# Optimization experiments

Measured on AMD Instinct MI355X. Metric: run time of the kernel, lower is better.

Reference implementation:

```python
import jax, jax.numpy as jnp
import numpy as np

# Gemma3 layer 0 (sliding-window layer -> local RoPE)
H = 8          # query heads
KVH = 4        # kv heads
DH = 256       # head dim
WINDOW = 1024  # sliding window
THETA_LOCAL = 10000.0
SCALE = 256.0 ** -0.5  # query_pre_attn_scalar**-0.5
EPS = 1e-6


def setup_inputs() -> dict:
    key = jax.random.key(0)
    ks = jax.random.split(key, 8)
    B, S, D = 1, 4096, 2560
    return {
        "hidden_states": jax.random.normal(ks[0], (B, S, D), jnp.float32),
        "attention_mask": jnp.ones((B, S), jnp.int32),
        "position_ids": jnp.broadcast_to(jnp.arange(S, dtype=jnp.int64), (B, S)),
        "wq": jax.random.normal(ks[1], (D, H * DH), jnp.float32) * 0.02,
        "wk": jax.random.normal(ks[2], (D, KVH * DH), jnp.float32) * 0.02,
        "wv": jax.random.normal(ks[3], (D, KVH * DH), jnp.float32) * 0.02,
        "wo": jax.random.normal(ks[4], (H * DH, D), jnp.float32) * 0.02,
        "q_norm_w": jnp.zeros((DH,), jnp.float32),  # Gemma RMSNorm uses (1 + w)
        "k_norm_w": jnp.zeros((DH,), jnp.float32),
    }


def _rms_norm(x, w):
    # Gemma-style RMSNorm over head_dim: x/rms * (1 + w)
    var = jnp.mean(jnp.square(x), axis=-1, keepdims=True)
    return x * jax.lax.rsqrt(var + EPS) * (1.0 + w)


def _rotate_half(x):
    x1, x2 = jnp.split(x, 2, axis=-1)
    return jnp.concatenate([-x2, x1], axis=-1)


def _rope(pos):
    # local RoPE (rope_type 'default', theta = rope_local_base_freq)
    inv_freq = 1.0 / (THETA_LOCAL ** (jnp.arange(0, DH, 2, dtype=jnp.float32) / DH))
    freqs = pos.astype(jnp.float32)[..., None] * inv_freq  # [B,S,DH/2]
    emb = jnp.concatenate([freqs, freqs], axis=-1)         # [B,S,DH]
    return jnp.cos(emb), jnp.sin(emb)


def reference(hidden_states, attention_mask, position_ids, wq, wk, wv, wo, q_norm_w, k_norm_w):
    B, S, D = hidden_states.shape
    # projections -> [B, heads, S, DH]
    q = (hidden_states @ wq).reshape(B, S, H, DH).transpose(0, 2, 1, 3)
    k = (hidden_states @ wk).reshape(B, S, KVH, DH).transpose(0, 2, 1, 3)
    v = (hidden_states @ wv).reshape(B, S, KVH, DH).transpose(0, 2, 1, 3)

    # per-head q/k RMSNorm (Gemma3)
    q = _rms_norm(q, q_norm_w)
    k = _rms_norm(k, k_norm_w)

    # RoPE
    cos, sin = _rope(position_ids)           # [B,S,DH]
    cos, sin = cos[:, None], sin[:, None]    # broadcast over heads
    q = q * cos + _rotate_half(q) * sin
    k = k * cos + _rotate_half(k) * sin

    # GQA: repeat kv heads
    rep = H // KVH
    k = jnp.repeat(k, rep, axis=1)
    v = jnp.repeat(v, rep, axis=1)

    # causal + sliding-window mask, combined with padding mask
    qi = jnp.arange(S)[:, None]
    ki = jnp.arange(S)[None, :]
    sw_mask = (ki <= qi) & (qi - ki < WINDOW)               # [S,S]
    pad = attention_mask.astype(bool)[:, None, None, :]     # [B,1,1,S]
    mask = sw_mask[None, None] & pad

    scores = jnp.einsum("bhqd,bhkd->bhqk", q, k) * SCALE
    scores = jnp.where(mask, scores, jnp.finfo(scores.dtype).min)
    probs = jax.nn.softmax(scores, axis=-1)

    out = jnp.einsum("bhqk,bhkd->bhqd", probs, v)            # [B,H,S,DH]
    out = out.transpose(0, 2, 1, 3).reshape(B, S, H * DH)
    return out @ wo
```

## Files before the change

kernel.cpp:

```cpp
#include <hip/hip_runtime.h>
#include <stdint.h>
#include <math.h>

typedef __bf16 bf16_t;
typedef __bf16 bf16x8 __attribute__((ext_vector_type(8)));
typedef __bf16 bf16x4 __attribute__((ext_vector_type(4)));
typedef float f32x4 __attribute__((ext_vector_type(4)));

#define GLD_LDS16(g, l)                                             \
    __builtin_amdgcn_global_load_lds(                               \
        (const __attribute__((address_space(1))) void*)(g),         \
        (__attribute__((address_space(3))) void*)(l), 16, 0, 0)

#define WAITV(N) asm volatile("s_waitcnt vmcnt(" #N ")" ::: "memory")
#define BARRIER() do { __builtin_amdgcn_sched_barrier(0);           \
                       __builtin_amdgcn_s_barrier();                \
                       __builtin_amdgcn_sched_barrier(0); } while (0)

__global__ __launch_bounds__(256)
void conv_bf16(const float* __restrict__ in, bf16_t* __restrict__ out, int n4)
{
    int i = blockIdx.x * 256 + threadIdx.x;
    if (i >= n4) return;
    float4 v = ((const float4*)in)[i];
    bf16x4 o = { (bf16_t)v.x, (bf16_t)v.y, (bf16_t)v.z, (bf16_t)v.w };
    ((bf16x4*)out)[i] = o;
}

__global__ __launch_bounds__(256)
void transpose_h(const float* __restrict__ in, bf16_t* __restrict__ out,
                 int R, int C)
{
    __shared__ float t[64][65];
    const int r0 = blockIdx.y * 64, c0 = blockIdx.x * 64;
#pragma unroll
    for (int i = 0; i < 16; ++i) {
        int f = threadIdx.x + i * 256;
        int r = f >> 6, c = f & 63;
        t[r][c] = in[(size_t)(r0 + r) * C + c0 + c];
    }
    __syncthreads();
#pragma unroll
    for (int i = 0; i < 16; ++i) {
        int f = threadIdx.x + i * 256;
        int r = f >> 6, c = f & 63;
        out[(size_t)(c0 + r) * R + r0 + c] = (bf16_t)t[c][r];
    }
}

__global__ __launch_bounds__(256)
void rope_tables(float* __restrict__ ct, float* __restrict__ st)
{
    int t = blockIdx.x * 256 + threadIdx.x;
    int s = t >> 7, j = t & 127;
    double inv = exp2((double)j * (-13.28771237954945 / 128.0));
    double ang = fmod((double)s * inv, 6.283185307179586476925286766559);
    ct[t] = (float)cos(ang);
    st[t] = (float)sin(ang);
}

__global__ __launch_bounds__(512, 2)
void gemm1(const bf16_t* __restrict__ A, const bf16_t* __restrict__ Bh,
           bf16_t* __restrict__ qb, bf16_t* __restrict__ kb,
           bf16_t* __restrict__ vt)
{
    __shared__ __attribute__((aligned(16))) char smem[131072];
    const int tid = threadIdx.x, lane = tid & 63, wid = tid >> 6;
    const int g = lane >> 4, c16 = lane & 15;
    const int wm = wid >> 2, wn = wid & 3;
    const int m0 = blockIdx.y * 256, n0 = blockIdx.x * 256;
    const int swz = c16 & 7;
    const int NT = 40;

    f32x4 acc[8][4];
#pragma unroll
    for (int m = 0; m < 8; ++m)
#pragma unroll
        for (int n = 0; n < 4; ++n) acc[m][n] = (f32x4)(0.f);

    auto STAGE_A = [&](int dbuf, int kt, int half) {
#pragma unroll
        for (int pl = 0; pl < 2; ++pl) {
            int c = pl * 512 + tid;
            int row = c >> 3, b = c & 7;
            GLD_LDS16(A + (size_t)(m0 + half * 128 + row) * 2560 + kt * 64
                        + ((b ^ (row & 7)) << 3),
                      smem + dbuf * 65536 + half * 16384
                        + (pl * 512 + wid * 64) * 16);
        }
    };
    auto STAGE_B = [&](int dbuf, int kt, int qp) {
#pragma unroll
        for (int pl = 0; pl < 2; ++pl) {
            int c = pl * 512 + tid;
            int u = c >> 3, b = c & 7;
            int row = ((u >> 5) << 6) + qp * 32 + (u & 31);
            int u0 = pl * 64 + wid * 8;
            int row0 = ((u0 >> 5) << 6) + qp * 32 + (u0 & 31);
            GLD_LDS16(Bh + (size_t)(n0 + row) * 2560 + kt * 64
                        + ((b ^ (row & 7)) << 3),
                      smem + dbuf * 65536 + 32768 + row0 * 128);
        }
    };

    STAGE_A(0, 0, 0); STAGE_A(0, 0, 1); STAGE_B(0, 0, 0); STAGE_B(0, 0, 1);
    WAITV(2);
    BARRIER();

    for (int t = 0; t < NT; ++t) {
        const int buf = t & 1, nbuf = buf ^ 1;
        const char* Ab = smem + buf * 65536;
        const char* Bb = smem + buf * 65536 + 32768;
        auto rdA = [&](int m, int kk) {
            return *(const bf16x8*)(Ab + (wm * 128 + m * 16 + c16) * 128
                                       + (((kk * 4 + g) ^ swz) << 4));
        };
        auto rdB = [&](int n, int kk) {
            return *(const bf16x8*)(Bb + (wn * 64 + n * 16 + c16) * 128
                                       + (((kk * 4 + g) ^ swz) << 4));
        };
        bf16x8 a[8], b0, b1, b2, b3;

#pragma unroll
        for (int m = 0; m < 8; ++m) a[m] = rdA(m, 0);
        b0 = rdB(0, 0); b1 = rdB(1, 0);
        if (t + 1 < NT) STAGE_A(nbuf, t + 1, 0);
        BARRIER();
        __builtin_amdgcn_s_setprio(1);
#pragma unroll
        for (int m = 0; m < 8; ++m) {
            acc[m][0] = __builtin_amdgcn_mfma_f32_16x16x32_bf16(a[m], b0, acc[m][0], 0, 0, 0);
            acc[m][1] = __builtin_amdgcn_mfma_f32_16x16x32_bf16(a[m], b1, acc[m][1], 0, 0, 0);
        }
        __builtin_amdgcn_s_setprio(0);
        if (t + 1 < NT) { WAITV(2); } else { WAITV(0); }
        BARRIER();

        b2 = rdB(2, 0); b3 = rdB(3, 0);
        if (t + 1 < NT) STAGE_A(nbuf, t + 1, 1);
        BARRIER();
        __builtin_amdgcn_s_setprio(1);
#pragma unroll
        for (int m = 0; m < 8; ++m) {
            acc[m][2] = __builtin_amdgcn_mfma_f32_16x16x32_bf16(a[m], b2, acc[m][2], 0, 0, 0);
            acc[m][3] = __builtin_amdgcn_mfma_f32_16x16x32_bf16(a[m], b3, acc[m][3], 0, 0, 0);
        }
        __builtin_amdgcn_s_setprio(0);
        BARRIER();

#pragma unroll
        for (int m = 0; m < 8; ++m) a[m] = rdA(m, 1);
        b0 = rdB(0, 1); b1 = rdB(1, 1);
        if (t + 1 < NT) STAGE_B(nbuf, t + 1, 0);
        BARRIER();
        __builtin_amdgcn_s_setprio(1);
#pragma unroll
        for (int m = 0; m < 8; ++m) {
            acc[m][0] = __builtin_amdgcn_mfma_f32_16x16x32_bf16(a[m], b0, acc[m][0], 0, 0, 0);
            acc[m][1] = __builtin_amdgcn_mfma_f32_16x16x32_bf16(a[m], b1, acc[m][1], 0, 0, 0);
        }
        __builtin_amdgcn_s_setprio(0);
        BARRIER();

        b2 = rdB(2, 1); b3 = rdB(3, 1);
        if (t + 1 < NT) STAGE_B(nbuf, t + 1, 1);
        BARRIER();
        __builtin_amdgcn_s_setprio(1);
#pragma unroll
        for (int m = 0; m < 8; ++m) {
            acc[m][2] = __builtin_amdgcn_mfma_f32_16x16x32_bf16(a[m], b2, acc[m][2], 0, 0, 0);
            acc[m][3] = __builtin_amdgcn_mfma_f32_16x16x32_bf16(a[m], b3, acc[m][3], 0, 0, 0);
        }
        __builtin_amdgcn_s_setprio(0);
        if (t + 1 < NT) WAITV(2);
        BARRIER();
    }

    if (n0 < 2048) {
#pragma unroll
        for (int m = 0; m < 8; ++m)
#pragma unroll
            for (int n = 0; n < 4; ++n) {
                int col = n0 + wn * 64 + n * 16 + c16;
                int rowb = m0 + wm * 128 + m * 16 + g * 4;
#pragma unroll
                for (int r = 0; r < 4; ++r)
                    qb[(size_t)(rowb + r) * 2048 + col] = (bf16_t)acc[m][n][r];
            }
    } else if (n0 < 3072) {
#pragma unroll
        for (int m = 0; m < 8; ++m)
#pragma unroll
            for (int n = 0; n < 4; ++n) {
                int col = n0 + wn * 64 + n * 16 + c16 - 2048;
                int rowb = m0 + wm * 128 + m * 16 + g * 4;
#pragma unroll
                for (int r = 0; r < 4; ++r)
                    kb[(size_t)(rowb + r) * 1024 + col] = (bf16_t)acc[m][n][r];
            }
    } else {
#pragma unroll
        for (int m = 0; m < 8; ++m)
#pragma unroll
            for (int n = 0; n < 4; ++n) {
                int d = n0 + wn * 64 + n * 16 + c16 - 3072;
                int rowb = m0 + wm * 128 + m * 16 + g * 4;
                int kvh_ = d >> 8, dd = d & 255;
                int kt = rowb >> 5, key = rowb & 31;
                bf16x4 hv;
#pragma unroll
                for (int r = 0; r < 4; ++r) hv[r] = (bf16_t)acc[m][n][r];
                size_t off = (size_t)kvh_ * 1048576 + (size_t)kt * 8192
                           + dd * 32 + (((key >> 3) ^ (dd & 3)) << 3) + (key & 7);
                *(bf16x4*)(vt + off) = hv;
            }
    }
}

__global__ __launch_bounds__(512, 2)
void gemm2p(const bf16_t* __restrict__ A, const bf16_t* __restrict__ Bh,
            float* __restrict__ C)
{
    __shared__ __attribute__((aligned(16))) char smem[131072];
    const int tid = threadIdx.x, lane = tid & 63, wid = tid >> 6;
    const int g = lane >> 4, c16 = lane & 15;
    const int wm = wid >> 2, wn = wid & 3;
    const int m0 = blockIdx.y * 256, n0 = blockIdx.x * 256;
    const int swz = c16 & 7;
    const int NT = 32;

    f32x4 acc[8][4];
#pragma unroll
    for (int m = 0; m < 8; ++m)
#pragma unroll
        for (int n = 0; n < 4; ++n) acc[m][n] = (f32x4)(0.f);

    auto STAGE_A = [&](int dbuf, int kt, int half) {
#pragma unroll
        for (int pl = 0; pl < 2; ++pl) {
            int c = pl * 512 + tid;
            int row = c >> 3, b = c & 7;
            GLD_LDS16(A + (size_t)(m0 + half * 128 + row) * 2048 + kt * 64
                        + ((b ^ (row & 7)) << 3),
                      smem + dbuf * 65536 + half * 16384
                        + (pl * 512 + wid * 64) * 16);
        }
    };
    auto STAGE_B = [&](int dbuf, int kt, int qp) {
#pragma unroll
        for (int pl = 0; pl < 2; ++pl) {
            int c = pl * 512 + tid;
            int u = c >> 3, b = c & 7;
            int row = ((u >> 5) << 6) + qp * 32 + (u & 31);
            int u0 = pl * 64 + wid * 8;
            int row0 = ((u0 >> 5) << 6) + qp * 32 + (u0 & 31);
            GLD_LDS16(Bh + (size_t)(n0 + row) * 2048 + kt * 64
                        + ((b ^ (row & 7)) << 3),
                      smem + dbuf * 65536 + 32768 + row0 * 128);
        }
    };

    STAGE_A(0, 0, 0); STAGE_A(0, 0, 1); STAGE_B(0, 0, 0); STAGE_B(0, 0, 1);
    WAITV(2);
    BARRIER();

    for (int t = 0; t < NT; ++t) {
        const int buf = t & 1, nbuf = buf ^ 1;
        const char* Ab = smem + buf * 65536;
        const char* Bb = smem + buf * 65536 + 32768;
        auto rdA = [&](int m, int kk) {
            return *(const bf16x8*)(Ab + (wm * 128 + m * 16 + c16) * 128
                                       + (((kk * 4 + g) ^ swz) << 4));
        };
        auto rdB = [&](int n, int kk) {
            return *(const bf16x8*)(Bb + (wn * 64 + n * 16 + c16) * 128
                                       + (((kk * 4 + g) ^ swz) << 4));
        };
        bf16x8 a[8], b0, b1, b2, b3;

#pragma unroll
        for (int m = 0; m < 8; ++m) a[m] = rdA(m, 0);
        b0 = rdB(0, 0); b1 = rdB(1, 0);
        if (t + 1 < NT) STAGE_A(nbuf, t + 1, 0);
        BARRIER();
        __builtin_amdgcn_s_setprio(1);
#pragma unroll
        for (int m = 0; m < 8; ++m) {
            acc[m][0] = __builtin_amdgcn_mfma_f32_16x16x32_bf16(a[m], b0, acc[m][0], 0, 0, 0);
            acc[m][1] = __builtin_amdgcn_mfma_f32_16x16x32_bf16(a[m], b1, acc[m][1], 0, 0, 0);
        }
        __builtin_amdgcn_s_setprio(0);
        if (t + 1 < NT) { WAITV(2); } else { WAITV(0); }
        BARRIER();

        b2 = rdB(2, 0); b3 = rdB(3, 0);
        if (t + 1 < NT) STAGE_A(nbuf, t + 1, 1);
        BARRIER();
        __builtin_amdgcn_s_setprio(1);
#pragma unroll
        for (int m = 0; m < 8; ++m) {
            acc[m][2] = __builtin_amdgcn_mfma_f32_16x16x32_bf16(a[m], b2, acc[m][2], 0, 0, 0);
            acc[m][3] = __builtin_amdgcn_mfma_f32_16x16x32_bf16(a[m], b3, acc[m][3], 0, 0, 0);
        }
        __builtin_amdgcn_s_setprio(0);
        BARRIER();

#pragma unroll
        for (int m = 0; m < 8; ++m) a[m] = rdA(m, 1);
        b0 = rdB(0, 1); b1 = rdB(1, 1);
        if (t + 1 < NT) STAGE_B(nbuf, t + 1, 0);
        BARRIER();
        __builtin_amdgcn_s_setprio(1);
#pragma unroll
        for (int m = 0; m < 8; ++m) {
            acc[m][0] = __builtin_amdgcn_mfma_f32_16x16x32_bf16(a[m], b0, acc[m][0], 0, 0, 0);
            acc[m][1] = __builtin_amdgcn_mfma_f32_16x16x32_bf16(a[m], b1, acc[m][1], 0, 0, 0);
        }
        __builtin_amdgcn_s_setprio(0);
        BARRIER();

        b2 = rdB(2, 1); b3 = rdB(3, 1);
        if (t + 1 < NT) STAGE_B(nbuf, t + 1, 1);
        BARRIER();
        __builtin_amdgcn_s_setprio(1);
#pragma unroll
        for (int m = 0; m < 8; ++m) {
            acc[m][2] = __builtin_amdgcn_mfma_f32_16x16x32_bf16(a[m], b2, acc[m][2], 0, 0, 0);
            acc[m][3] = __builtin_amdgcn_mfma_f32_16x16x32_bf16(a[m], b3, acc[m][3], 0, 0, 0);
        }
        __builtin_amdgcn_s_setprio(0);
        if (t + 1 < NT) WAITV(2);
        BARRIER();
    }

#pragma unroll
    for (int m = 0; m < 8; ++m)
#pragma unroll
        for (int n = 0; n < 4; ++n) {
            int col = n0 + wn * 64 + n * 16 + c16;
            int rowb = m0 + wm * 128 + m * 16 + g * 4;
#pragma unroll
            for (int r = 0; r < 4; ++r)
                C[(size_t)(rowb + r) * 2560 + col] = acc[m][n][r];
        }
}

__global__ __launch_bounds__(256)
void norm_q(bf16_t* __restrict__ qb, const float* __restrict__ w,
            const float* __restrict__ ct, const float* __restrict__ st)
{
    const int s = blockIdx.x, t = threadIdx.x;
    const int h = t >> 5, l = t & 31;
    bf16_t* base = qb + (size_t)s * 2048 + h * 256 + l * 8;
    bf16x8 hv = *(const bf16x8*)base;
    float x[8], ss = 0.f;
#pragma unroll
    for (int j = 0; j < 8; ++j) { x[j] = (float)hv[j]; ss += x[j] * x[j]; }
#pragma unroll
    for (int mk = 1; mk < 32; mk <<= 1) ss += __shfl_xor(ss, mk);
    const float rs = rsqrtf(ss * (1.f / 256.f) + 1e-6f);
    float4 w0 = *(const float4*)(w + l * 8);
    float4 w1 = *(const float4*)(w + l * 8 + 4);
    float wa[8] = { w0.x, w0.y, w0.z, w0.w, w1.x, w1.y, w1.z, w1.w };
    float xn[8];
#pragma unroll
    for (int j = 0; j < 8; ++j) xn[j] = x[j] * rs * (1.f + wa[j]);
    const int d0 = (l * 8) & 127;
    float4 c0 = *(const float4*)(ct + s * 128 + d0);
    float4 c1 = *(const float4*)(ct + s * 128 + d0 + 4);
    float4 s0 = *(const float4*)(st + s * 128 + d0);
    float4 s1 = *(const float4*)(st + s * 128 + d0 + 4);
    float cc[8] = { c0.x, c0.y, c0.z, c0.w, c1.x, c1.y, c1.z, c1.w };
    float sn[8] = { s0.x, s0.y, s0.z, s0.w, s1.x, s1.y, s1.z, s1.w };
    const bool upper = (l >= 16);
    bf16x8 oh;
#pragma unroll
    for (int j = 0; j < 8; ++j) {
        float pn = __shfl_xor(xn[j], 16);
        float rot = upper ? pn : -pn;
        oh[j] = (bf16_t)(xn[j] * cc[j] + rot * sn[j]);
    }
    *(bf16x8*)base = oh;
}

__global__ __launch_bounds__(256)
void norm_k(const bf16_t* __restrict__ kraw, bf16_t* __restrict__ kb2,
            const float* __restrict__ w, const float* __restrict__ ct,
            const float* __restrict__ st)
{
    const int s = blockIdx.x, t = threadIdx.x;
    const int h = t >> 6, l = t & 63;
    const bf16_t* base = kraw + (size_t)s * 1024 + h * 256 + l * 4;
    bf16x4 hv = *(const bf16x4*)base;
    float x[4], ss = 0.f;
#pragma unroll
    for (int j = 0; j < 4; ++j) { x[j] = (float)hv[j]; ss += x[j] * x[j]; }
#pragma unroll
    for (int mk = 1; mk < 64; mk <<= 1) ss += __shfl_xor(ss, mk);
    const float rs = rsqrtf(ss * (1.f / 256.f) + 1e-6f);
    float4 w0 = *(const float4*)(w + l * 4);
    float wa[4] = { w0.x, w0.y, w0.z, w0.w };
    float xn[4];
#pragma unroll
    for (int j = 0; j < 4; ++j) xn[j] = x[j] * rs * (1.f + wa[j]);
    const int d0 = (l * 4) & 127;
    float4 c0 = *(const float4*)(ct + s * 128 + d0);
    float4 s0 = *(const float4*)(st + s * 128 + d0);
    float cc[4] = { c0.x, c0.y, c0.z, c0.w };
    float sn[4] = { s0.x, s0.y, s0.z, s0.w };
    const bool upper = (l >= 32);
    bf16x4 oh;
#pragma unroll
    for (int j = 0; j < 4; ++j) {
        float pn = __shfl_xor(xn[j], 32);
        float rot = upper ? pn : -pn;
        oh[j] = (bf16_t)(xn[j] * cc[j] + rot * sn[j]);
    }
    bf16_t* dst = kb2 + (size_t)h * 1048576 + (size_t)(s >> 5) * 8192
                + (s & 31) * 256 + (((l >> 1) ^ (s & 7)) << 3) + (l & 1) * 4;
    *(bf16x4*)dst = oh;
}

__global__ __launch_bounds__(256)
void attn_fwd6(const bf16_t* __restrict__ qb, const bf16_t* __restrict__ kb2,
               const bf16_t* __restrict__ vt2, bf16_t* __restrict__ attn)
{
    __shared__ __attribute__((aligned(16))) char smem[2 * 32768];
    __shared__ __attribute__((aligned(16))) bf16_t P[4][16][40];
    const int tid = threadIdx.x, lane = tid & 63, wid = tid >> 6;
    const int g = lane >> 4, c16 = lane & 15;
    const int h = blockIdx.x, kvh = h >> 1;
    const int by = blockIdx.y;
    const int qt = (by & 1) ? (63 - (by >> 1)) : (by >> 1);
    const int qrow0 = qt * 64 + wid * 16;

    const char* kslab = (const char*)kb2 + (size_t)kvh * 2097152;
    const char* vslab = (const char*)vt2 + (size_t)kvh * 2097152;

    bf16x8 qf[8];
#pragma unroll
    for (int c = 0; c < 8; ++c)
        qf[c] = *(const bf16x8*)(qb + (size_t)(qrow0 + c16) * 2048 + h * 256 + c * 32 + g * 8);

    float lrow[4] = { 0.f, 0.f, 0.f, 0.f };
    f32x4 acc[16];
#pragma unroll
    for (int nd = 0; nd < 16; ++nd) acc[nd] = (f32x4)(0.f);

    auto STAGE = [&](int buf, int kt) {
        char* Kd = smem + buf * 32768;
        char* Vd = smem + buf * 32768 + 16384;
        const char* ks = kslab + (size_t)kt * 16384;
        const char* vs = vslab + (size_t)kt * 16384;
#pragma unroll
        for (int j = 0; j < 4; ++j)
            GLD_LDS16(ks + (size_t)(j * 256 + tid) * 16, Kd + (j * 256 + wid * 64) * 16);
#pragma unroll
        for (int j = 0; j < 4; ++j)
            GLD_LDS16(vs + (size_t)(j * 256 + tid) * 16, Vd + (j * 256 + wid * 64) * 16);
    };

    const int ktb_lo = (qt >= 16) ? 2 * qt - 32 : 0;
    const int ktb_hi = 2 * qt + 1;
    int cur = 0;
    STAGE(0, ktb_lo);
    __syncthreads();

    const int swk = (c16 & 7) << 4;
    const int swv = (g ^ (c16 & 3)) << 4;
    const float S2 = 0.090168441f;

    for (int kt = ktb_lo; kt <= ktb_hi; ++kt) {
        if (kt < ktb_hi) STAGE(cur ^ 1, kt + 1);

        if (kt * 32 <= qrow0 + 15 && kt * 32 + 31 >= qrow0 - 1023) {
            const char* Kc = smem + cur * 32768;
            const char* Vc = smem + cur * 32768 + 16384;

            f32x4 scA[2], scB[2];
#pragma unroll
            for (int n = 0; n < 2; ++n) { scA[n] = (f32x4)(0.f); scB[n] = (f32x4)(0.f); }
            __builtin_amdgcn_s_setprio(1);
#pragma unroll
            for (int n = 0; n < 2; ++n) {
                const char* kr = Kc + (n * 16 + c16) * 512;
#pragma unroll
                for (int c = 0; c < 4; ++c) {
                    bf16x8 kf = *(const bf16x8*)(kr + ((((c * 4 + g) << 4) ^ swk)));
                    scA[n] = __builtin_amdgcn_mfma_f32_16x16x32_bf16(qf[c], kf, scA[n], 0, 0, 0);
                }
#pragma unroll
                for (int c = 4; c < 8; ++c) {
                    bf16x8 kf = *(const bf16x8*)(kr + ((((c * 4 + g) << 4) ^ swk)));
                    scB[n] = __builtin_amdgcn_mfma_f32_16x16x32_bf16(qf[c], kf, scB[n], 0, 0, 0);
                }
            }
            __builtin_amdgcn_s_setprio(0);

            float p2[2][4];
            const bool fullv = (kt * 32 + 31 <= qrow0) && (kt * 32 >= qrow0 - 1008);
            if (fullv) {
#pragma unroll
                for (int n = 0; n < 2; ++n)
#pragma unroll
                    for (int r = 0; r < 4; ++r)
                        p2[n][r] = __builtin_amdgcn_exp2f((scA[n][r] + scB[n][r]) * S2);
            } else {
#pragma unroll
                for (int n = 0; n < 2; ++n) {
                    const int key = kt * 32 + n * 16 + c16;
#pragma unroll
                    for (int r = 0; r < 4; ++r) {
                        const int q = qrow0 + g * 4 + r;
                        bool valid = (key <= q) && (q - key < 1024);
                        float e = __builtin_amdgcn_exp2f((scA[n][r] + scB[n][r]) * S2);
                        p2[n][r] = valid ? e : 0.f;
                    }
                }
            }
#pragma unroll
            for (int n = 0; n < 2; ++n)
#pragma unroll
                for (int r = 0; r < 4; ++r) lrow[r] += p2[n][r];

#pragma unroll
            for (int n = 0; n < 2; ++n)
#pragma unroll
                for (int r = 0; r < 4; ++r)
                    P[wid][g * 4 + r][n * 16 + c16] = (bf16_t)p2[n][r];
            bf16x8 pa = *(const bf16x8*)(&P[wid][c16][g * 8]);
            __builtin_amdgcn_s_setprio(1);
#pragma unroll
            for (int nd = 0; nd < 16; ++nd) {
                bf16x8 vf = *(const bf16x8*)(Vc + (nd * 16 + c16) * 64 + swv);
                acc[nd] = __builtin_amdgcn_mfma_f32_16x16x32_bf16(pa, vf, acc[nd], 0, 0, 0);
            }
            __builtin_amdgcn_s_setprio(0);
        }
        __syncthreads();
        cur ^= 1;
    }

#pragma unroll
    for (int mk = 1; mk < 16; mk <<= 1)
#pragma unroll
        for (int r = 0; r < 4; ++r) lrow[r] += __shfl_xor(lrow[r], mk);

    float inv[4];
#pragma unroll
    for (int r = 0; r < 4; ++r) inv[r] = 1.f / lrow[r];
#pragma unroll
    for (int nd = 0; nd < 16; ++nd)
#pragma unroll
        for (int r = 0; r < 4; ++r) {
            int row = qrow0 + g * 4 + r;
            attn[(size_t)row * 2048 + h * 256 + nd * 16 + c16] =
                (bf16_t)(acc[nd][r] * inv[r]);
        }
}

extern "C" void kernel_launch(void* const* d_in, const int* in_sizes, int n_in,
                              void* d_out, int out_size, void* d_ws, size_t ws_size,
                              hipStream_t stream)
{
    (void)in_sizes; (void)n_in; (void)out_size; (void)ws_size;
    const float* hs  = (const float*)d_in[0];
    const float* wq  = (const float*)d_in[3];
    const float* wk  = (const float*)d_in[4];
    const float* wv  = (const float*)d_in[5];
    const float* wo  = (const float*)d_in[6];
    const float* qnw = (const float*)d_in[7];
    const float* knw = (const float*)d_in[8];

    char* ws = (char*)d_ws;
    bf16_t* hs_bf = (bf16_t*)(ws);
    bf16_t* qb    = (bf16_t*)(ws + 20971520);
    bf16_t* kraw  = (bf16_t*)(ws + 37748736);
    bf16_t* vt2   = (bf16_t*)(ws + 46137344);
    bf16_t* Bh    = (bf16_t*)(ws + 54525952);
    bf16_t* kb2   = (bf16_t*)(ws + 54525952);
    float*  ct    = (float*)(ws + 75497472);
    float*  st    = (float*)(ws + 77594624);
    bf16_t* attnb = (bf16_t*)(ws);
    bf16_t* woh   = (bf16_t*)(ws + 20971520);

    conv_bf16<<<10240, 256, 0, stream>>>(hs, hs_bf, 4096 * 2560 / 4);
    transpose_h<<<dim3(32, 40), 256, 0, stream>>>(wq, Bh, 2560, 2048);
    transpose_h<<<dim3(16, 40), 256, 0, stream>>>(wk, Bh + (size_t)2048 * 2560, 2560, 1024);
    transpose_h<<<dim3(16, 40), 256, 0, stream>>>(wv, Bh + (size_t)3072 * 2560, 2560, 1024);

    gemm1<<<dim3(16, 16), 512, 0, stream>>>(hs_bf, Bh, qb, kraw, vt2);

    rope_tables<<<2048, 256, 0, stream>>>(ct, st);
    norm_q<<<4096, 256, 0, stream>>>(qb, qnw, ct, st);
    norm_k<<<4096, 256, 0, stream>>>(kraw, kb2, knw, ct, st);

    attn_fwd6<<<dim3(8, 64), 256, 0, stream>>>(qb, kb2, vt2, attnb);

    transpose_h<<<dim3(40, 32), 256, 0, stream>>>(wo, woh, 2048, 2560);
    gemm2p<<<dim3(10, 16), 512, 0, stream>>>(attnb, woh, (float*)d_out);
}
```

Before: 243.9 us.

## Fuse prep and q/k norm kernels, issue GEMM tile loads earlier

The two GEMMs now issue the A and B global-to-LDS loads for the next k-tile together in the first two phases of each iteration, instead of spreading them over all four. The vmcnt waits are adjusted to match, which aims to hide more memory latency behind the MFMA work. The bf16 conversion and the three weight transposes are merged into one `prep` launch, and `norm_q` and `norm_k` become a single 512-thread kernel, which removes several small launches. `rope_tables` now runs before `gemm1`. Issuing more loads in flight at once raises pressure on the memory system and changes the overlap between loads and MFMA work.

```diff
diff --git a/kernel.cpp b/kernel.cpp
--- a/kernel.cpp
+++ b/kernel.cpp
@@ -18,13 +18,38 @@
                        __builtin_amdgcn_sched_barrier(0); } while (0)
 
 __global__ __launch_bounds__(256)
-void conv_bf16(const float* __restrict__ in, bf16_t* __restrict__ out, int n4)
-{
-    int i = blockIdx.x * 256 + threadIdx.x;
-    if (i >= n4) return;
-    float4 v = ((const float4*)in)[i];
-    bf16x4 o = { (bf16_t)v.x, (bf16_t)v.y, (bf16_t)v.z, (bf16_t)v.w };
-    ((bf16x4*)out)[i] = o;
+void prep(const float* __restrict__ hs, bf16_t* __restrict__ hsb,
+          const float* __restrict__ wq, const float* __restrict__ wk,
+          const float* __restrict__ wv, bf16_t* __restrict__ Bh)
+{
+    const int b = blockIdx.x;
+    if (b >= 2560) {
+        int i = (b - 2560) * 256 + threadIdx.x;
+        float4 v = ((const float4*)hs)[i];
+        bf16x4 o = { (bf16_t)v.x, (bf16_t)v.y, (bf16_t)v.z, (bf16_t)v.w };
+        ((bf16x4*)hsb)[i] = o;
+        return;
+    }
+    const float* src; bf16_t* dst; int C, bx, by;
+    if (b < 1280)      { src = wq; dst = Bh;                          C = 2048; bx = b % 32;          by = b / 32; }
+    else if (b < 1920) { src = wk; dst = Bh + (size_t)2048 * 2560;    C = 1024; bx = (b - 1280) % 16; by = (b - 1280) / 16; }
+    else               { src = wv; dst = Bh + (size_t)3072 * 2560;    C = 1024; bx = (b - 1920) % 16; by = (b - 1920) / 16; }
+    const int R = 2560;
+    __shared__ float t[64][65];
+    const int r0 = by * 64, c0 = bx * 64;
+#pragma unroll
+    for (int i = 0; i < 16; ++i) {
+        int f = threadIdx.x + i * 256;
+        int r = f >> 6, c = f & 63;
+        t[r][c] = src[(size_t)(r0 + r) * C + c0 + c];
+    }
+    __syncthreads();
+#pragma unroll
+    for (int i = 0; i < 16; ++i) {
+        int f = threadIdx.x + i * 256;
+        int r = f >> 6, c = f & 63;
+        dst[(size_t)(c0 + r) * R + r0 + c] = (bf16_t)t[c][r];
+    }
 }
 
 __global__ __launch_bounds__(256)
@@ -103,7 +128,7 @@
         }
     };
 
-    STAGE_A(0, 0, 0); STAGE_A(0, 0, 1); STAGE_B(0, 0, 0); STAGE_B(0, 0, 1);
+    STAGE_A(0, 0, 0); STAGE_B(0, 0, 0); STAGE_A(0, 0, 1); STAGE_B(0, 0, 1);
     WAITV(2);
     BARRIER();
 
@@ -124,7 +149,7 @@
 #pragma unroll
         for (int m = 0; m < 8; ++m) a[m] = rdA(m, 0);
         b0 = rdB(0, 0); b1 = rdB(1, 0);
-        if (t + 1 < NT) STAGE_A(nbuf, t + 1, 0);
+        if (t + 1 < NT) { STAGE_A(nbuf, t + 1, 0); STAGE_B(nbuf, t + 1, 0); }
         BARRIER();
         __builtin_amdgcn_s_setprio(1);
 #pragma unroll
@@ -133,11 +158,11 @@
             acc[m][1] = __builtin_amdgcn_mfma_f32_16x16x32_bf16(a[m], b1, acc[m][1], 0, 0, 0);
         }
         __builtin_amdgcn_s_setprio(0);
-        if (t + 1 < NT) { WAITV(2); } else { WAITV(0); }
+        if (t + 1 < NT) { WAITV(4); } else { WAITV(0); }
         BARRIER();
 
         b2 = rdB(2, 0); b3 = rdB(3, 0);
-        if (t + 1 < NT) STAGE_A(nbuf, t + 1, 1);
+        if (t + 1 < NT) { STAGE_A(nbuf, t + 1, 1); STAGE_B(nbuf, t + 1, 1); }
         BARRIER();
         __builtin_amdgcn_s_setprio(1);
 #pragma unroll
@@ -151,7 +176,6 @@
 #pragma unroll
         for (int m = 0; m < 8; ++m) a[m] = rdA(m, 1);
         b0 = rdB(0, 1); b1 = rdB(1, 1);
-        if (t + 1 < NT) STAGE_B(nbuf, t + 1, 0);
         BARRIER();
         __builtin_amdgcn_s_setprio(1);
 #pragma unroll
@@ -163,7 +187,6 @@
         BARRIER();
 
         b2 = rdB(2, 1); b3 = rdB(3, 1);
-        if (t + 1 < NT) STAGE_B(nbuf, t + 1, 1);
         BARRIER();
         __builtin_amdgcn_s_setprio(1);
 #pragma unroll
@@ -260,7 +283,7 @@
         }
     };
 
-    STAGE_A(0, 0, 0); STAGE_A(0, 0, 1); STAGE_B(0, 0, 0); STAGE_B(0, 0, 1);
+    STAGE_A(0, 0, 0); STAGE_B(0, 0, 0); STAGE_A(0, 0, 1); STAGE_B(0, 0, 1);
     WAITV(2);
     BARRIER();
 
@@ -281,7 +304,7 @@
 #pragma unroll
         for (int m = 0; m < 8; ++m) a[m] = rdA(m, 0);
         b0 = rdB(0, 0); b1 = rdB(1, 0);
-        if (t + 1 < NT) STAGE_A(nbuf, t + 1, 0);
+        if (t + 1 < NT) { STAGE_A(nbuf, t + 1, 0); STAGE_B(nbuf, t + 1, 0); }
         BARRIER();
         __builtin_amdgcn_s_setprio(1);
 #pragma unroll
@@ -290,11 +313,11 @@
             acc[m][1] = __builtin_amdgcn_mfma_f32_16x16x32_bf16(a[m], b1, acc[m][1], 0, 0, 0);
         }
         __builtin_amdgcn_s_setprio(0);
-        if (t + 1 < NT) { WAITV(2); } else { WAITV(0); }
+        if (t + 1 < NT) { WAITV(4); } else { WAITV(0); }
         BARRIER();
 
         b2 = rdB(2, 0); b3 = rdB(3, 0);
-        if (t + 1 < NT) STAGE_A(nbuf, t + 1, 1);
+        if (t + 1 < NT) { STAGE_A(nbuf, t + 1, 1); STAGE_B(nbuf, t + 1, 1); }
         BARRIER();
         __builtin_amdgcn_s_setprio(1);
 #pragma unroll
@@ -308,7 +331,6 @@
 #pragma unroll
         for (int m = 0; m < 8; ++m) a[m] = rdA(m, 1);
         b0 = rdB(0, 1); b1 = rdB(1, 1);
-        if (t + 1 < NT) STAGE_B(nbuf, t + 1, 0);
         BARRIER();
         __builtin_amdgcn_s_setprio(1);
 #pragma unroll
@@ -320,7 +342,6 @@
         BARRIER();
 
         b2 = rdB(2, 1); b3 = rdB(3, 1);
-        if (t + 1 < NT) STAGE_B(nbuf, t + 1, 1);
         BARRIER();
         __builtin_amdgcn_s_setprio(1);
 #pragma unroll
@@ -345,80 +366,78 @@
         }
 }
 
-__global__ __launch_bounds__(256)
-void norm_q(bf16_t* __restrict__ qb, const float* __restrict__ w,
-            const float* __restrict__ ct, const float* __restrict__ st)
+__global__ __launch_bounds__(512)
+void norm_qk(bf16_t* __restrict__ qb, const bf16_t* __restrict__ kraw,
+             bf16_t* __restrict__ kb2, const float* __restrict__ qw,
+             const float* __restrict__ kw, const float* __restrict__ ct,
+             const float* __restrict__ st)
 {
     const int s = blockIdx.x, t = threadIdx.x;
-    const int h = t >> 5, l = t & 31;
-    bf16_t* base = qb + (size_t)s * 2048 + h * 256 + l * 8;
-    bf16x8 hv = *(const bf16x8*)base;
-    float x[8], ss = 0.f;
-#pragma unroll
-    for (int j = 0; j < 8; ++j) { x[j] = (float)hv[j]; ss += x[j] * x[j]; }
-#pragma unroll
-    for (int mk = 1; mk < 32; mk <<= 1) ss += __shfl_xor(ss, mk);
-    const float rs = rsqrtf(ss * (1.f / 256.f) + 1e-6f);
-    float4 w0 = *(const float4*)(w + l * 8);
-    float4 w1 = *(const float4*)(w + l * 8 + 4);
-    float wa[8] = { w0.x, w0.y, w0.z, w0.w, w1.x, w1.y, w1.z, w1.w };
-    float xn[8];
-#pragma unroll
-    for (int j = 0; j < 8; ++j) xn[j] = x[j] * rs * (1.f + wa[j]);
-    const int d0 = (l * 8) & 127;
-    float4 c0 = *(const float4*)(ct + s * 128 + d0);
-    float4 c1 = *(const float4*)(ct + s * 128 + d0 + 4);
-    float4 s0 = *(const float4*)(st + s * 128 + d0);
-    float4 s1 = *(const float4*)(st + s * 128 + d0 + 4);
-    float cc[8] = { c0.x, c0.y, c0.z, c0.w, c1.x, c1.y, c1.z, c1.w };
-    float sn[8] = { s0.x, s0.y, s0.z, s0.w, s1.x, s1.y, s1.z, s1.w };
-    const bool upper = (l >= 16);
-    bf16x8 oh;
-#pragma unroll
-    for (int j = 0; j < 8; ++j) {
-        float pn = __shfl_xor(xn[j], 16);
-        float rot = upper ? pn : -pn;
-        oh[j] = (bf16_t)(xn[j] * cc[j] + rot * sn[j]);
-    }
-    *(bf16x8*)base = oh;
-}
-
-__global__ __launch_bounds__(256)
-void norm_k(const bf16_t* __restrict__ kraw, bf16_t* __restrict__ kb2,
-            const float* __restrict__ w, const float* __restrict__ ct,
-            const float* __restrict__ st)
-{
-    const int s = blockIdx.x, t = threadIdx.x;
-    const int h = t >> 6, l = t & 63;
-    const bf16_t* base = kraw + (size_t)s * 1024 + h * 256 + l * 4;
-    bf16x4 hv = *(const bf16x4*)base;
-    float x[4], ss = 0.f;
-#pragma unroll
-    for (int j = 0; j < 4; ++j) { x[j] = (float)hv[j]; ss += x[j] * x[j]; }
-#pragma unroll
-    for (int mk = 1; mk < 64; mk <<= 1) ss += __shfl_xor(ss, mk);
-    const float rs = rsqrtf(ss * (1.f / 256.f) + 1e-6f);
-    float4 w0 = *(const float4*)(w + l * 4);
-    float wa[4] = { w0.x, w0.y, w0.z, w0.w };
-    float xn[4];
-#pragma unroll
-    for (int j = 0; j < 4; ++j) xn[j] = x[j] * rs * (1.f + wa[j]);
-    const int d0 = (l * 4) & 127;
-    float4 c0 = *(const float4*)(ct + s * 128 + d0);
-    float4 s0 = *(const float4*)(st + s * 128 + d0);
-    float cc[4] = { c0.x, c0.y, c0.z, c0.w };
-    float sn[4] = { s0.x, s0.y, s0.z, s0.w };
-    const bool upper = (l >= 32);
-    bf16x4 oh;
-#pragma unroll
-    for (int j = 0; j < 4; ++j) {
-        float pn = __shfl_xor(xn[j], 32);
-        float rot = upper ? pn : -pn;
-        oh[j] = (bf16_t)(xn[j] * cc[j] + rot * sn[j]);
-    }
-    bf16_t* dst = kb2 + (size_t)h * 1048576 + (size_t)(s >> 5) * 8192
-                + (s & 31) * 256 + (((l >> 1) ^ (s & 7)) << 3) + (l & 1) * 4;
-    *(bf16x4*)dst = oh;
+    if (t < 256) {
+        const int h = t >> 5, l = t & 31;
+        bf16_t* base = qb + (size_t)s * 2048 + h * 256 + l * 8;
+        bf16x8 hv = *(const bf16x8*)base;
+        float x[8], ss = 0.f;
+#pragma unroll
+        for (int j = 0; j < 8; ++j) { x[j] = (float)hv[j]; ss += x[j] * x[j]; }
+#pragma unroll
+        for (int mk = 1; mk < 32; mk <<= 1) ss += __shfl_xor(ss, mk);
+        const float rs = rsqrtf(ss * (1.f / 256.f) + 1e-6f);
+        float4 w0 = *(const float4*)(qw + l * 8);
+        float4 w1 = *(const float4*)(qw + l * 8 + 4);
+        float wa[8] = { w0.x, w0.y, w0.z, w0.w, w1.x, w1.y, w1.z, w1.w };
+        float xn[8];
+#pragma unroll
+        for (int j = 0; j < 8; ++j) xn[j] = x[j] * rs * (1.f + wa[j]);
+        const int d0 = (l * 8) & 127;
+        float4 c0 = *(const float4*)(ct + s * 128 + d0);
+        float4 c1 = *(const float4*)(ct + s * 128 + d0 + 4);
+        float4 s0 = *(const float4*)(st + s * 128 + d0);
+        float4 s1 = *(const float4*)(st + s * 128 + d0 + 4);
+        float cc[8] = { c0.x, c0.y, c0.z, c0.w, c1.x, c1.y, c1.z, c1.w };
+        float sn[8] = { s0.x, s0.y, s0.z, s0.w, s1.x, s1.y, s1.z, s1.w };
+        const bool upper = (l >= 16);
+        bf16x8 oh;
+#pragma unroll
+        for (int j = 0; j < 8; ++j) {
+            float pn = __shfl_xor(xn[j], 16);
+            float rot = upper ? pn : -pn;
+            oh[j] = (bf16_t)(xn[j] * cc[j] + rot * sn[j]);
+        }
+        *(bf16x8*)base = oh;
+    } else {
+        const int tk = t - 256;
+        const int h = tk >> 6, l = tk & 63;
+        const bf16_t* base = kraw + (size_t)s * 1024 + h * 256 + l * 4;
+        bf16x4 hv = *(const bf16x4*)base;
+        float x[4], ss = 0.f;
+#pragma unroll
+        for (int j = 0; j < 4; ++j) { x[j] = (float)hv[j]; ss += x[j] * x[j]; }
+#pragma unroll
+        for (int mk = 1; mk < 64; mk <<= 1) ss += __shfl_xor(ss, mk);
+        const float rs = rsqrtf(ss * (1.f / 256.f) + 1e-6f);
+        float4 w0 = *(const float4*)(kw + l * 4);
+        float wa[4] = { w0.x, w0.y, w0.z, w0.w };
+        float xn[4];
+#pragma unroll
+        for (int j = 0; j < 4; ++j) xn[j] = x[j] * rs * (1.f + wa[j]);
+        const int d0 = (l * 4) & 127;
+        float4 c0 = *(const float4*)(ct + s * 128 + d0);
+        float4 s0 = *(const float4*)(st + s * 128 + d0);
+        float cc[4] = { c0.x, c0.y, c0.z, c0.w };
+        float sn[4] = { s0.x, s0.y, s0.z, s0.w };
+        const bool upper = (l >= 32);
+        bf16x4 oh;
+#pragma unroll
+        for (int j = 0; j < 4; ++j) {
+            float pn = __shfl_xor(xn[j], 32);
+            float rot = upper ? pn : -pn;
+            oh[j] = (bf16_t)(xn[j] * cc[j] + rot * sn[j]);
+        }
+        bf16_t* dst = kb2 + (size_t)h * 1048576 + (size_t)(s >> 5) * 8192
+                    + (s & 31) * 256 + (((l >> 1) ^ (s & 7)) << 3) + (l & 1) * 4;
+        *(bf16x4*)dst = oh;
+    }
 }
 
 __global__ __launch_bounds__(256)
@@ -584,16 +603,12 @@
     bf16_t* attnb = (bf16_t*)(ws);
     bf16_t* woh   = (bf16_t*)(ws + 20971520);
 
-    conv_bf16<<<10240, 256, 0, stream>>>(hs, hs_bf, 4096 * 2560 / 4);
-    transpose_h<<<dim3(32, 40), 256, 0, stream>>>(wq, Bh, 2560, 2048);
-    transpose_h<<<dim3(16, 40), 256, 0, stream>>>(wk, Bh + (size_t)2048 * 2560, 2560, 1024);
-    transpose_h<<<dim3(16, 40), 256, 0, stream>>>(wv, Bh + (size_t)3072 * 2560, 2560, 1024);
+    prep<<<12800, 256, 0, stream>>>(hs, hs_bf, wq, wk, wv, Bh);
+    rope_tables<<<2048, 256, 0, stream>>>(ct, st);
 
     gemm1<<<dim3(16, 16), 512, 0, stream>>>(hs_bf, Bh, qb, kraw, vt2);
 
-    rope_tables<<<2048, 256, 0, stream>>>(ct, st);
-    norm_q<<<4096, 256, 0, stream>>>(qb, qnw, ct, st);
-    norm_k<<<4096, 256, 0, stream>>>(kraw, kb2, knw, ct, st);
+    norm_qk<<<4096, 512, 0, stream>>>(qb, kraw, kb2, qnw, knw, ct, st);
 
     attn_fwd6<<<dim3(8, 64), 256, 0, stream>>>(qb, kb2, vt2, attnb);
 
```

After: 239.6 us. About the same (-1.7%).
